# Performance work log

Hardware: AMD Instinct MI355X
Metric: run time of the kernel (lower is better)

## Reference

```python
import jax, jax.numpy as jnp
import numpy as np

B, S, D, H = 1, 2048, 1024, 16
HD = D // H  # head_dim = 64


def _split_heads(x):
    # [B,S,D] -> [B,H,S,HD]
    return x.reshape(B, S, H, HD).transpose(0, 2, 1, 3)


def setup_inputs() -> dict:
    key = jax.random.key(0)
    ks = jax.random.split(key, 8)
    p = 0.02
    return {
        "hidden_states": jax.random.normal(ks[0], (B, S, D), jnp.float32),
        "knowledge": jax.random.normal(ks[1], (B, S, D), jnp.float32),
        "Wq": jax.random.normal(ks[2], (2 * D, D), jnp.float32) * p,
        "Wk_know": jax.random.normal(ks[3], (D, D), jnp.float32) * p,
        "Wk_mlp": jax.random.normal(ks[4], (D, D), jnp.float32) * p,
        "Wv_know": jax.random.normal(ks[5], (D, D), jnp.float32) * p,
        "Wv_mlp": jax.random.normal(ks[6], (D, D), jnp.float32) * p,
        "Wo": jax.random.normal(ks[7], (D, D), jnp.float32) * p,
    }


def reference(hidden_states, knowledge, Wq, Wk_know, Wk_mlp, Wv_know, Wv_mlp, Wo):
    shared = jnp.concatenate([hidden_states, knowledge], axis=-1)  # [B,S,2D]
    q = _split_heads(shared @ Wq)            # [B,H,S,HD]
    k_know = _split_heads(knowledge @ Wk_know)
    k_mlp = _split_heads(hidden_states @ Wk_mlp)
    v_know = _split_heads(knowledge @ Wv_know)
    v_mlp = _split_heads(hidden_states @ Wv_mlp)

    scale = jnp.asarray(D, jnp.float32) ** 0.5  # note: full embed_dim, not head_dim
    mask_value = jnp.finfo(jnp.float32).min
    causal = jnp.tril(jnp.ones((S, S), dtype=bool))  # [S,S]

    s_know = jnp.einsum("bhqd,bhkd->bhqk", q, k_know) / scale
    s_know = jnp.where(causal, s_know, mask_value)
    s_mlp = jnp.einsum("bhqd,bhkd->bhqk", q, k_mlp) / scale
    s_mlp = jnp.where(causal, s_mlp, mask_value)

    concat_scores = jax.nn.softmax(jnp.concatenate([s_know, s_mlp], axis=-1), axis=-1)  # [B,H,S,2S]
    concat_values = jnp.concatenate([v_know, v_mlp], axis=-2)  # [B,H,2S,HD]
    out = jnp.einsum("bhqk,bhkd->bhqd", concat_scores, concat_values)
    out = out.transpose(0, 2, 1, 3).reshape(B, S, D) @ Wo  # merge heads + proj_o
    return out, concat_scores
```

## Files before the change

### kernel.cpp

```cpp
#include <hip/hip_runtime.h>

typedef unsigned short u16;
typedef float f32x4 __attribute__((ext_vector_type(4)));
typedef __bf16 bf16x8 __attribute__((ext_vector_type(8)));
typedef unsigned int u32x4 __attribute__((ext_vector_type(4)));
typedef u16 u16x4 __attribute__((ext_vector_type(4)));

#define S_ 2048
#define D_ 1024
#define H_ 16
#define HD_ 64

#define WAITV(N) asm volatile("s_waitcnt vmcnt(" #N ")" ::: "memory")
#define BAR() __builtin_amdgcn_s_barrier()
#define SFENCE() __builtin_amdgcn_sched_barrier(0)

__device__ __forceinline__ u16 f2bf(float f) {
  unsigned int u = __builtin_bit_cast(unsigned int, f);
  u += 0x7fffu + ((u >> 16) & 1u);
  return (u16)(u >> 16);
}

__device__ __forceinline__ f32x4 mfma16(bf16x8 a, bf16x8 b, f32x4 c) {
  return __builtin_amdgcn_mfma_f32_16x16x32_bf16(a, b, c, 0, 0, 0);
}

__device__ __forceinline__ float ex2(float x) {
  float r;
  asm("v_exp_f32 %0, %1\n\ts_nop 1" : "=v"(r) : "v"(x));
  return r;
}

__device__ __forceinline__ void gld_lds16(const u16* g, u16* l) {
  __builtin_amdgcn_global_load_lds((const __attribute__((address_space(1))) void*)g,
                                   (__attribute__((address_space(3))) void*)l, 16, 0, 0);
}

__global__ __launch_bounds__(256) void prep_kernel(
    const float* __restrict__ hs, const float* __restrict__ kn, const float* __restrict__ Wq,
    const float* __restrict__ Wkk, const float* __restrict__ Wvk, const float* __restrict__ Wkm,
    const float* __restrict__ Wvm, const float* __restrict__ Wo, u16* __restrict__ hs_bf,
    u16* __restrict__ kn_bf, u16* __restrict__ WqT, u16* __restrict__ WkvkT,
    u16* __restrict__ WkvmT, u16* __restrict__ WoT, int n4) {
  __shared__ float tile[32][33];
  int b = blockIdx.x;
  if (b < 4096) {
    int i = b * 256 + threadIdx.x;
    const float* s;
    u16* d;
    int j;
    if (i < n4) { s = hs; d = hs_bf; j = i; }
    else { j = i - n4; if (j >= n4) return; s = kn; d = kn_bf; }
    f32x4 v = *(const f32x4*)(s + (size_t)j * 4);
    u16x4 o;
    o[0] = f2bf(v[0]); o[1] = f2bf(v[1]); o[2] = f2bf(v[2]); o[3] = f2bf(v[3]);
    *(u16x4*)(d + (size_t)j * 4) = o;
    return;
  }
  int idx = b - 4096;
  int bc = idx & 31, y = idx >> 5;
  const float* W;
  u16* WT;
  int R, br;
  const size_t HM = (size_t)1024 * 1024;
  if (y < 64) { W = Wq; WT = WqT; R = 2048; br = y; }
  else {
    R = 1024; br = y & 31;
    switch ((y - 64) >> 5) {
      case 0: W = Wkk; WT = WkvkT; break;
      case 1: W = Wvk; WT = WkvkT + HM; break;
      case 2: W = Wkm; WT = WkvmT; break;
      case 3: W = Wvm; WT = WkvmT + HM; break;
      default: W = Wo; WT = WoT; break;
    }
  }
  int tx = threadIdx.x & 31, ty = threadIdx.x >> 5;
#pragma unroll
  for (int i = 0; i < 4; ++i)
    tile[ty + i * 8][tx] = W[(size_t)(br * 32 + ty + i * 8) * 1024 + bc * 32 + tx];
  __syncthreads();
#pragma unroll
  for (int i = 0; i < 4; ++i)
    WT[(size_t)(bc * 32 + ty + i * 8) * R + br * 32 + tx] = f2bf(tile[tx][ty + i * 8]);
}

template <int MODE, int MI, int NI>
__device__ __forceinline__ void gemm_body(u16* smem, const u16* A0, const u16* A1, int ksplit,
                                          const u16* BT, void* Cp, int K, int ldc, int bn,
                                          int bm) {
  constexpr int BM = MI * 32, BN = NI * 32;
  u16* const As0 = smem;
  u16* const Bs0 = smem + 2 * BM * 32;
  const int tid = threadIdx.x, l = tid & 63, w = tid >> 6;
  const int wm = w >> 1, wn = w & 1;
  f32x4 zf = {0.f, 0.f, 0.f, 0.f};
  f32x4 acc[MI][NI];
#pragma unroll
  for (int mi = 0; mi < MI; ++mi)
#pragma unroll
    for (int ni = 0; ni < NI; ++ni) acc[mi][ni] = zf;

  auto STAGE = [&](int b, int t) {
    int k0 = t * 32;
#pragma unroll
    for (int i = 0; i < MI / 2; ++i) {
      int idx = tid + i * 256, r = idx >> 2, c = idx & 3;
      int sc = c ^ ((r >> 1) & 3);
      int k = k0 + sc * 8;
      const u16* src = (k < ksplit) ? (A0 + (size_t)(bm * BM + r) * D_ + k)
                                    : (A1 + (size_t)(bm * BM + r) * D_ + (k - ksplit));
      gld_lds16(src, As0 + b * BM * 32 + idx * 8);
    }
#pragma unroll
    for (int i = 0; i < NI / 2; ++i) {
      int idx = tid + i * 256, r = idx >> 2, c = idx & 3;
      int sc = c ^ ((r >> 1) & 3);
      gld_lds16(BT + (size_t)(bn * BN + r) * K + k0 + sc * 8, Bs0 + b * BN * 32 + idx * 8);
    }
  };

  const int nt = K >> 5;
  STAGE(0, 0);
  int cur = 0;
  for (int t = 0; t < nt; ++t) {
    if (t + 1 < nt) {
      STAGE(cur ^ 1, t + 1);
      if constexpr (MI + NI == 8) { WAITV(4); }
      else if constexpr (MI + NI == 6) { WAITV(3); }
      else { WAITV(2); }
    } else {
      WAITV(0);
    }
    BAR(); SFENCE();
    const u16* Asc = As0 + cur * BM * 32;
    const u16* Bsc = Bs0 + cur * BN * 32;
    bf16x8 af[MI], bfr[NI];
#pragma unroll
    for (int mi = 0; mi < MI; ++mi) {
      int row = wm * (MI * 16) + mi * 16 + (l & 15);
      int slot = (l >> 4) ^ ((row >> 1) & 3);
      af[mi] = __builtin_bit_cast(bf16x8, *(const u32x4*)(Asc + row * 32 + slot * 8));
    }
#pragma unroll
    for (int ni = 0; ni < NI; ++ni) {
      int row = wn * (NI * 16) + ni * 16 + (l & 15);
      int slot = (l >> 4) ^ ((row >> 1) & 3);
      bfr[ni] = __builtin_bit_cast(bf16x8, *(const u32x4*)(Bsc + row * 32 + slot * 8));
    }
#pragma unroll
    for (int mi = 0; mi < MI; ++mi)
#pragma unroll
      for (int ni = 0; ni < NI; ++ni) acc[mi][ni] = mfma16(af[mi], bfr[ni], acc[mi][ni]);
    SFENCE(); BAR();
    cur ^= 1;
  }

  if constexpr (MODE == 2) {
#pragma unroll
    for (int mi = 0; mi < MI; ++mi)
#pragma unroll
      for (int ni = 0; ni < NI; ++ni) {
        u16x4 pk;
#pragma unroll
        for (int r = 0; r < 4; ++r) pk[r] = f2bf(acc[mi][ni][r]);
        int n = bn * BN + wn * (NI * 16) + ni * 16 + (l & 15);
        int m0 = bm * BM + wm * (MI * 16) + mi * 16 + (l >> 4) * 4;
        *(u16x4*)((u16*)Cp + (size_t)n * S_ + m0) = pk;
      }
  } else if constexpr (MODE == 0) {
    __syncthreads();
    u16* Cs = smem;
#pragma unroll
    for (int mi = 0; mi < MI; ++mi)
#pragma unroll
      for (int ni = 0; ni < NI; ++ni)
#pragma unroll
        for (int r = 0; r < 4; ++r) {
          int row = wm * (MI * 16) + mi * 16 + (l >> 4) * 4 + r;
          int col = wn * (NI * 16) + ni * 16 + (l & 15);
          Cs[row * 144 + col] = f2bf(acc[mi][ni][r]);
        }
    __syncthreads();
    constexpr int CPR = BN / 8;
#pragma unroll
    for (int i = 0; i < BM * CPR / 256; ++i) {
      int idx = tid + i * 256;
      int lr = idx / CPR, cc = idx % CPR;
      u32x4 v = *(const u32x4*)(Cs + lr * 144 + cc * 8);
      *(u32x4*)((u16*)Cp + (size_t)(bm * BM + lr) * ldc + bn * BN + cc * 8) = v;
    }
  } else {
    __syncthreads();
    float* Cs = (float*)smem;
#pragma unroll
    for (int mi = 0; mi < MI; ++mi)
#pragma unroll
      for (int ni = 0; ni < NI; ++ni)
#pragma unroll
        for (int r = 0; r < 4; ++r) {
          int row = wm * (MI * 16) + mi * 16 + (l >> 4) * 4 + r;
          int col = wn * (NI * 16) + ni * 16 + (l & 15);
          Cs[row * 136 + col] = acc[mi][ni][r];
        }
    __syncthreads();
    constexpr int CPR = BN / 4;
#pragma unroll
    for (int i = 0; i < BM * CPR / 256; ++i) {
      int idx = tid + i * 256;
      int lr = idx / CPR, cc = idx % CPR;
      f32x4 v = *(const f32x4*)(Cs + lr * 136 + cc * 4);
      __builtin_nontemporal_store(v, (f32x4*)((float*)Cp + (size_t)(bm * BM + lr) * ldc +
                                              bn * BN + cc * 4));
    }
  }
}

__global__ __launch_bounds__(256) void proj_gemm(const u16* __restrict__ hs_bf,
                                                 const u16* __restrict__ kn_bf,
                                                 const u16* __restrict__ WqT,
                                                 const u16* __restrict__ WkvkT,
                                                 const u16* __restrict__ WkvmT,
                                                 u16* __restrict__ qb, u16* __restrict__ kk,
                                                 u16* __restrict__ km, u16* __restrict__ vkT,
                                                 u16* __restrict__ vmT) {
  __shared__ __attribute__((aligned(16))) u16 smem[18432];
  int bid = blockIdx.x;
  int xcd = bid & 7, ixd = bid >> 3;
  int bm, bn;
  if (ixd < 16) {
    bm = xcd * 2 + (ixd >> 3);
    bn = ixd & 7;
  } else if (ixd >= 64 && ixd < 80) {
    return;
  } else {
    int s = (ixd < 64) ? (ixd - 16) : (48 + (ixd - 80));
    bm = xcd * 2 + (s >> 5);
    bn = 8 + (s & 31);
  }
  const size_t HM = (size_t)1024 * 1024;
  const int BIG = 1 << 30;
  if (bn < 8) {
    gemm_body<0, 4, 4>(smem, hs_bf, kn_bf, 1024, WqT, qb, 2048, 1024, bn, bm);
  } else if (bn < 16) {
    gemm_body<0, 4, 4>(smem, kn_bf, kn_bf, BIG, WkvkT, kk, 1024, 1024, bn - 8, bm);
  } else if (bn < 24) {
    gemm_body<2, 4, 4>(smem, kn_bf, kn_bf, BIG, WkvkT + HM, vkT, 1024, 0, bn - 16, bm);
  } else if (bn < 32) {
    gemm_body<0, 4, 4>(smem, hs_bf, hs_bf, BIG, WkvmT, km, 1024, 1024, bn - 24, bm);
  } else {
    gemm_body<2, 4, 4>(smem, hs_bf, hs_bf, BIG, WkvmT + HM, vmT, 1024, 0, bn - 32, bm);
  }
}

__global__ __launch_bounds__(256) void out_gemm(const u16* __restrict__ aob,
                                                const u16* __restrict__ WoT,
                                                float* __restrict__ out) {
  __shared__ __attribute__((aligned(16))) u16 smem[17408];
  int bid = blockIdx.x;
  int xcd = bid & 7, i = bid >> 3;
  int bm = xcd * 4 + (i >> 4), bn = i & 15;
  gemm_body<1, 2, 2>(smem, aob, aob, 1 << 30, WoT, out, 1024, 1024, bn, bm);
}

__device__ __forceinline__ void stage_async64_t512(u16* dst, const u16* src, int stride,
                                                   int tid) {
  int ci = tid;
  int r = ci >> 3, c = ci & 7;
  int sc = c ^ (r & 7);
  gld_lds16(src + (size_t)r * stride + sc * 8, dst + ci * 8);
}

__device__ __forceinline__ bf16x8 ld_frag64(const u16* lds, int rowbase, int chunkbase, int l) {
  int row = rowbase + (l & 15);
  int chunk = chunkbase + (l >> 4);
  int slot = chunk ^ (row & 7);
  return __builtin_bit_cast(bf16x8, *(const u32x4*)(lds + row * 64 + slot * 8));
}

__global__ __launch_bounds__(512) void attn_kernel(const u16* __restrict__ qb,
                                                   const u16* __restrict__ kk,
                                                   const u16* __restrict__ km,
                                                   const u16* __restrict__ vkT,
                                                   const u16* __restrict__ vmT,
                                                   float* __restrict__ scores,
                                                   u16* __restrict__ ao) {
  const int fid = blockIdx.x;
  const int xcd = fid & 7, ixd = fid >> 3;
  const int h = xcd * 2 + (ixd >> 5);
  const int j = ixd & 31;
  const int a = j >> 1;
  const int qt = (((j & 1) ^ (ixd >> 5)) == 0) ? (31 - a) : a;
  const int tid = threadIdx.x, w = tid >> 6, l = tid & 63;
  const int wk = w & 3, kh = w >> 2;
  const int nt = qt + 1;
  const int NT = 2 * nt;
  const int qrow0 = qt * 64;
  const int q16 = l & 15, c4 = l >> 4;
  const int qme = qrow0 + wk * 16 + q16;
  const float sc2 = 0.04508422f;

  __shared__ u16 kr[4][64 * 64];
  __shared__ u16 vr[4][64 * 64];
  __shared__ u16 ps[64 * 64];
  __shared__ float stat[128];

  auto kptr = [&](int it) {
    int hf = it >= nt;
    int t = it - (hf ? nt : 0);
    const u16* kb = hf ? km : kk;
    return kb + (size_t)(t * 64) * 1024 + h * HD_;
  };
  auto vptr = [&](int it) {
    int hf = it >= nt;
    int t = it - (hf ? nt : 0);
    const u16* vb = hf ? vmT : vkT;
    return vb + (size_t)(h * HD_) * S_ + t * 64;
  };

  {
    int r = tid >> 3, c = tid & 7;
    u32x4 v = *(const u32x4*)(qb + (size_t)(qrow0 + r) * D_ + h * HD_ + c * 8);
    *(u32x4*)(ps + r * 64 + ((c ^ (r & 7)) * 8)) = v;
  }
  __syncthreads();
  bf16x8 qA0 = ld_frag64(ps, wk * 16, 0, l);
  bf16x8 qA1 = ld_frag64(ps, wk * 16, 4, l);
  __syncthreads();

  float aa[4] = {0.f, 0.f, 0.f, 0.f};
  stage_async64_t512(kr[0], kptr(0), 1024, tid);
  stage_async64_t512(kr[1], kptr(1), 1024, tid);
  for (int p = 0; p < NT; p += 2) {
    WAITV(0);
    BAR(); SFENCE();
    if (p + 2 < NT) {
      stage_async64_t512(kr[(p + 2) & 3], kptr(p + 2), 1024, tid);
      stage_async64_t512(kr[(p + 3) & 3], kptr(p + 3), 1024, tid);
    }
    __builtin_amdgcn_s_setprio(1);
#pragma unroll
    for (int half = 0; half < 2; ++half) {
      int it = p + half;
      const u16* ksb = kr[it & 3];
      int domask = (it == nt - 1) || (it == NT - 1);
      int tbase = (it - (it >= nt ? nt : 0)) * 64;
      f32x4 zfv = {0.f, 0.f, 0.f, 0.f};
#pragma unroll
      for (int jf = 0; jf < 2; ++jf) {
        int kf = kh * 2 + jf;
        f32x4 z = zfv;
        z = mfma16(ld_frag64(ksb, kf * 16, 0, l), qA0, z);
        z = mfma16(ld_frag64(ksb, kf * 16, 4, l), qA1, z);
#pragma unroll
        for (int r = 0; r < 4; ++r) {
          float v = z[r];
          if (domask) {
            int key = tbase + kf * 16 + c4 * 4 + r;
            if (key > qme) v = -1e30f;
          }
          aa[r] += ex2(v * sc2);
        }
      }
    }
    __builtin_amdgcn_s_setprio(0);
    SFENCE();
  }
  float psum = (aa[0] + aa[1]) + (aa[2] + aa[3]);
  psum += __shfl_xor(psum, 16, 64);
  psum += __shfl_xor(psum, 32, 64);
  if (l < 16) stat[w * 16 + l] = psum;
  __syncthreads();
  const float lsum = stat[wk * 16 + q16] + stat[(wk + 4) * 16 + q16];
  const float moff = __log2f(lsum);

  f32x4 zf = {0.f, 0.f, 0.f, 0.f};
  f32x4 o[4];
#pragma unroll
  for (int df = 0; df < 4; ++df) o[df] = zf;

  float* const srow0 = scores + ((size_t)h * S_ + qme) * (2 * S_) + c4 * 4;
  const int prow = wk * 16 + q16;
  const int swz8 = (q16 & 7) << 1;

  stage_async64_t512(kr[0], kptr(0), 1024, tid);
  stage_async64_t512(kr[1], kptr(1), 1024, tid);
  stage_async64_t512(vr[0], vptr(0), S_, tid);
  stage_async64_t512(vr[1], vptr(1), S_, tid);
  for (int p = 0; p < NT; p += 2) {
    if (p == 0) { WAITV(0); } else { WAITV(4); }
    BAR(); SFENCE();
    if (p + 2 < NT) {
      stage_async64_t512(kr[(p + 2) & 3], kptr(p + 2), 1024, tid);
      stage_async64_t512(kr[(p + 3) & 3], kptr(p + 3), 1024, tid);
      stage_async64_t512(vr[(p + 2) & 3], vptr(p + 2), S_, tid);
      stage_async64_t512(vr[(p + 3) & 3], vptr(p + 3), S_, tid);
    }
#pragma unroll
    for (int half = 0; half < 2; ++half) {
      int it = p + half;
      int domask = (it == nt - 1) || (it == NT - 1);
      int hf = it >= nt;
      int tbase = (it - (hf ? nt : 0)) * 64;
      float pv[8];
      __builtin_amdgcn_s_setprio(1);
#pragma unroll
      for (int jf = 0; jf < 2; ++jf) {
        int kf = kh * 2 + jf;
        f32x4 z = zf;
        z = mfma16(ld_frag64(kr[it & 3], kf * 16, 0, l), qA0, z);
        z = mfma16(ld_frag64(kr[it & 3], kf * 16, 4, l), qA1, z);
#pragma unroll
        for (int r = 0; r < 4; ++r) {
          float v = z[r];
          if (domask) {
            int key = tbase + kf * 16 + c4 * 4 + r;
            if (key > qme) v = -1e30f;
          }
          pv[jf * 4 + r] = ex2(__builtin_fmaf(v, sc2, -moff));
        }
      }
      __builtin_amdgcn_s_setprio(0);
      float* srow = srow0 + hf * S_ + tbase;
#pragma unroll
      for (int jf = 0; jf < 2; ++jf) {
        int kf = kh * 2 + jf;
        f32x4 s4 = {pv[jf * 4], pv[jf * 4 + 1], pv[jf * 4 + 2], pv[jf * 4 + 3]};
        *(f32x4*)(srow + kf * 16) = s4;
      }
#pragma unroll
      for (int jf = 0; jf < 2; ++jf) {
        int kf = kh * 2 + jf;
        u16x4 pk;
#pragma unroll
        for (int r = 0; r < 4; ++r) pk[r] = f2bf(pv[jf * 4 + r]);
        int slot8 = (kf * 4 + c4) ^ swz8;
        *(u16x4*)(ps + prow * 64 + slot8 * 4) = pk;
      }
      __builtin_amdgcn_s_setprio(1);
      {
        bf16x8 pa = ld_frag64(ps, wk * 16, kh * 4, l);
#pragma unroll
        for (int df = 0; df < 4; ++df)
          o[df] = mfma16(ld_frag64(vr[it & 3], df * 16, kh * 4, l), pa, o[df]);
      }
      __builtin_amdgcn_s_setprio(0);
    }
    SFENCE();
  }

  __syncthreads();
  float* obuf = (float*)kr;
  if (kh == 1) {
#pragma unroll
    for (int df = 0; df < 4; ++df)
#pragma unroll
      for (int r = 0; r < 4; ++r)
        obuf[((wk * 4 + df) * 16 + c4 * 4 + r) * 16 + q16] = o[df][r];
  }
  __syncthreads();
  if (kh == 0) {
#pragma unroll
    for (int df = 0; df < 4; ++df) {
      u16x4 pk;
#pragma unroll
      for (int r = 0; r < 4; ++r) {
        float t = o[df][r] + obuf[((wk * 4 + df) * 16 + c4 * 4 + r) * 16 + q16];
        pk[r] = f2bf(t);
      }
      *(u16x4*)(ao + (size_t)qme * D_ + h * HD_ + df * 16 + c4 * 4) = pk;
    }
  }

  int zc = 2048 - nt * 64;
  if (zc > 0) {
    int vph = zc >> 2;
    f32x4 zero = {0.f, 0.f, 0.f, 0.f};
    float* base = scores + ((size_t)h * S_ + qrow0) * (2 * S_) + nt * 64;
    for (int row = 0; row < 64; ++row) {
      float* rp = base + (size_t)row * (2 * S_);
      for (int i = tid; i < vph; i += 512)
        __builtin_nontemporal_store(zero, (f32x4*)(rp + i * 4));
      for (int i = tid; i < vph; i += 512)
        __builtin_nontemporal_store(zero, (f32x4*)(rp + S_ + i * 4));
    }
  }
}

extern "C" void kernel_launch(void* const* d_in, const int* in_sizes, int n_in, void* d_out,
                              int out_size, void* d_ws, size_t ws_size, hipStream_t stream) {
  const float* hs = (const float*)d_in[0];
  const float* kn = (const float*)d_in[1];
  const float* Wq = (const float*)d_in[2];
  const float* Wkk = (const float*)d_in[3];
  const float* Wkm = (const float*)d_in[4];
  const float* Wvk = (const float*)d_in[5];
  const float* Wvm = (const float*)d_in[6];
  const float* Wo = (const float*)d_in[7];
  float* out = (float*)d_out;
  float* scores = out + (size_t)S_ * D_;

  const size_t M2 = (size_t)S_ * D_;
  u16* ws = (u16*)d_ws;
  u16* hs_bf = ws;
  u16* kn_bf = hs_bf + M2;
  u16* WqT = kn_bf + M2;
  u16* WkvkT = WqT + M2;
  u16* WkvmT = WkvkT + M2;
  u16* WoT = WkvmT + M2;
  u16* qb = WoT + M2 / 2;
  u16* kk = qb + M2;
  u16* km = kk + M2;
  u16* vkT = km + M2;
  u16* vmT = vkT + M2;
  u16* aob = vmT + M2;

  int n4 = (int)(M2 / 4);
  prep_kernel<<<11264, 256, 0, stream>>>(hs, kn, Wq, Wkk, Wvk, Wkm, Wvm, Wo, hs_bf, kn_bf, WqT,
                                         WkvkT, WkvmT, WoT, n4);
  proj_gemm<<<768, 256, 0, stream>>>(hs_bf, kn_bf, WqT, WkvkT, WkvmT, qb, kk, km, vkT, vmT);
  attn_kernel<<<512, 512, 0, stream>>>(qb, kk, km, vkT, vmT, scores, aob);
  out_gemm<<<512, 256, 0, stream>>>(aob, WoT, out);
}
```

Measured before the change: 180.6 us.

## Deepen K prefetch in stats pass and interleave masked-zero stores into PV loop

Merges the K and V LDS buffers into one array so the first (row-sum) pass can prefetch K tiles four ahead across six slots instead of two. It also moves the zeroing of the upper-triangle score region out of the tail and spreads it across the second loop's iterations, with each block zeroing tiles belonging to the complementary query tile (31-qt). This is meant to overlap the large zero-fill store traffic with compute and balance store work between short and long blocks. The cost is more in-flight memory operations, changed vmcnt wait counts that must stay correct, and a cross-block ownership scheme for the zero-fill.

```diff
diff --git a/kernel.cpp b/kernel.cpp
--- a/kernel.cpp
+++ b/kernel.cpp
@@ -299,8 +299,7 @@
   const int qme = qrow0 + wk * 16 + q16;
   const float sc2 = 0.04508422f;
 
-  __shared__ u16 kr[4][64 * 64];
-  __shared__ u16 vr[4][64 * 64];
+  __shared__ u16 krv[8 * 4096];
   __shared__ u16 ps[64 * 64];
   __shared__ float stat[128];
 
@@ -328,20 +327,19 @@
   __syncthreads();
 
   float aa[4] = {0.f, 0.f, 0.f, 0.f};
-  stage_async64_t512(kr[0], kptr(0), 1024, tid);
-  stage_async64_t512(kr[1], kptr(1), 1024, tid);
+#pragma unroll
+  for (int t = 0; t < 4; ++t)
+    if (t < NT) stage_async64_t512(krv + (t % 6) * 4096, kptr(t), 1024, tid);
   for (int p = 0; p < NT; p += 2) {
-    WAITV(0);
+    if (p + 2 < NT) { WAITV(2); } else { WAITV(0); }
     BAR(); SFENCE();
-    if (p + 2 < NT) {
-      stage_async64_t512(kr[(p + 2) & 3], kptr(p + 2), 1024, tid);
-      stage_async64_t512(kr[(p + 3) & 3], kptr(p + 3), 1024, tid);
-    }
+    if (p + 4 < NT) stage_async64_t512(krv + ((p + 4) % 6) * 4096, kptr(p + 4), 1024, tid);
+    if (p + 5 < NT) stage_async64_t512(krv + ((p + 5) % 6) * 4096, kptr(p + 5), 1024, tid);
     __builtin_amdgcn_s_setprio(1);
 #pragma unroll
     for (int half = 0; half < 2; ++half) {
       int it = p + half;
-      const u16* ksb = kr[it & 3];
+      const u16* ksb = krv + (it % 6) * 4096;
       int domask = (it == nt - 1) || (it == NT - 1);
       int tbase = (it - (it >= nt ? nt : 0)) * 64;
       f32x4 zfv = {0.f, 0.f, 0.f, 0.f};
@@ -381,19 +379,35 @@
   float* const srow0 = scores + ((size_t)h * S_ + qme) * (2 * S_) + c4 * 4;
   const int prow = wk * 16 + q16;
   const int swz8 = (q16 & 7) << 1;
-
-  stage_async64_t512(kr[0], kptr(0), 1024, tid);
-  stage_async64_t512(kr[1], kptr(1), 1024, tid);
-  stage_async64_t512(vr[0], vptr(0), S_, tid);
-  stage_async64_t512(vr[1], vptr(1), S_, tid);
+  const int rt = 31 - qt;
+
+  stage_async64_t512(krv + 0 * 4096, kptr(0), 1024, tid);
+  stage_async64_t512(krv + 1 * 4096, kptr(1), 1024, tid);
+  stage_async64_t512(krv + 4 * 4096, vptr(0), S_, tid);
+  stage_async64_t512(krv + 5 * 4096, vptr(1), S_, tid);
   for (int p = 0; p < NT; p += 2) {
-    if (p == 0) { WAITV(0); } else { WAITV(4); }
+    if (p == 0) { WAITV(0); } else { WAITV(8); }
     BAR(); SFENCE();
     if (p + 2 < NT) {
-      stage_async64_t512(kr[(p + 2) & 3], kptr(p + 2), 1024, tid);
-      stage_async64_t512(kr[(p + 3) & 3], kptr(p + 3), 1024, tid);
-      stage_async64_t512(vr[(p + 2) & 3], vptr(p + 2), S_, tid);
-      stage_async64_t512(vr[(p + 3) & 3], vptr(p + 3), S_, tid);
+      stage_async64_t512(krv + ((p + 2) & 3) * 4096, kptr(p + 2), 1024, tid);
+      stage_async64_t512(krv + ((p + 3) & 3) * 4096, kptr(p + 3), 1024, tid);
+      stage_async64_t512(krv + (4 + ((p + 2) & 3)) * 4096, vptr(p + 2), S_, tid);
+      stage_async64_t512(krv + (4 + ((p + 3) & 3)) * 4096, vptr(p + 3), S_, tid);
+    }
+    if (qt > 0) {
+      int pp = p >> 1;
+      if (pp >= qt) pp = qt - 1;
+      int col0 = (rt + 1) * 64 + pp * 64;
+      float* zb = scores + ((size_t)h * S_ + rt * 64) * (2 * S_) + col0;
+      f32x4 zero = {0.f, 0.f, 0.f, 0.f};
+      int idx = tid * 4;
+#pragma unroll
+      for (int e = 0; e < 4; ++e) {
+        int id = idx + e;
+        int row = id >> 5, rem = id & 31, hf2 = rem >> 4, cv = rem & 15;
+        __builtin_nontemporal_store(zero,
+                                    (f32x4*)(zb + (size_t)row * (2 * S_) + hf2 * S_ + cv * 4));
+      }
     }
 #pragma unroll
     for (int half = 0; half < 2; ++half) {
@@ -407,8 +421,8 @@
       for (int jf = 0; jf < 2; ++jf) {
         int kf = kh * 2 + jf;
         f32x4 z = zf;
-        z = mfma16(ld_frag64(kr[it & 3], kf * 16, 0, l), qA0, z);
-        z = mfma16(ld_frag64(kr[it & 3], kf * 16, 4, l), qA1, z);
+        z = mfma16(ld_frag64(krv + (it & 3) * 4096, kf * 16, 0, l), qA0, z);
+        z = mfma16(ld_frag64(krv + (it & 3) * 4096, kf * 16, 4, l), qA1, z);
 #pragma unroll
         for (int r = 0; r < 4; ++r) {
           float v = z[r];
@@ -441,7 +455,7 @@
         bf16x8 pa = ld_frag64(ps, wk * 16, kh * 4, l);
 #pragma unroll
         for (int df = 0; df < 4; ++df)
-          o[df] = mfma16(ld_frag64(vr[it & 3], df * 16, kh * 4, l), pa, o[df]);
+          o[df] = mfma16(ld_frag64(krv + (4 + (it & 3)) * 4096, df * 16, kh * 4, l), pa, o[df]);
       }
       __builtin_amdgcn_s_setprio(0);
     }
@@ -449,7 +463,7 @@
   }
 
   __syncthreads();
-  float* obuf = (float*)kr;
+  float* obuf = (float*)krv;
   if (kh == 1) {
 #pragma unroll
     for (int df = 0; df < 4; ++df)
@@ -468,20 +482,6 @@
         pk[r] = f2bf(t);
       }
       *(u16x4*)(ao + (size_t)qme * D_ + h * HD_ + df * 16 + c4 * 4) = pk;
-    }
-  }
-
-  int zc = 2048 - nt * 64;
-  if (zc > 0) {
-    int vph = zc >> 2;
-    f32x4 zero = {0.f, 0.f, 0.f, 0.f};
-    float* base = scores + ((size_t)h * S_ + qrow0) * (2 * S_) + nt * 64;
-    for (int row = 0; row < 64; ++row) {
-      float* rp = base + (size_t)row * (2 * S_);
-      for (int i = tid; i < vph; i += 512)
-        __builtin_nontemporal_store(zero, (f32x4*)(rp + i * 4));
-      for (int i = tid; i < vph; i += 512)
-        __builtin_nontemporal_store(zero, (f32x4*)(rp + S_ + i * 4));
     }
   }
 }
```

Result: slower. 517.6 us (+186.7%).
